# Kernel tuning notes

Measured on AMD Instinct MI355X. Metric: run time of the kernel, lower is better.

The kernel has to match this reference:

```python
import jax, jax.numpy as jnp
import numpy as np

NUM_HEADS = 16
ROPE_BASE = 10000.0


def _rope_interleaved(x, cos, sin):
    # x: (B, S, H, hd); cos/sin: (1, S, 1, hd//2)
    x1 = x[..., ::2]
    x2 = x[..., 1::2]
    r1 = x1 * cos - x2 * sin
    r2 = x1 * sin + x2 * cos
    return jnp.stack([r1, r2], axis=-1).reshape(x.shape)


def _rope_tables(seq_len, head_dim, dtype):
    dim = head_dim // 2
    freqs = jnp.exp(-jnp.arange(0, dim, dtype=dtype) * jnp.log(jnp.asarray(ROPE_BASE, dtype)) / dim)
    pos = jnp.arange(seq_len, dtype=dtype)
    angles = pos[:, None] * freqs[None, :]  # (S, hd//2)
    return jnp.cos(angles)[None, :, None, :], jnp.sin(angles)[None, :, None, :]


def setup_inputs() -> dict:
    key = jax.random.key(0)
    ks = jax.random.split(key, 9)
    B, S, D = 2, 2048, 2048
    sc = 1.0 / np.sqrt(D)
    return {
        "x": jax.random.normal(ks[0], (B, S, D), jnp.float32),
        "wq": jax.random.normal(ks[1], (D, D), jnp.float32) * sc,
        "bq": jax.random.normal(ks[2], (D,), jnp.float32) * 0.01,
        "wk": jax.random.normal(ks[3], (D, D), jnp.float32) * sc,
        "bk": jax.random.normal(ks[4], (D,), jnp.float32) * 0.01,
        "wv": jax.random.normal(ks[5], (D, D), jnp.float32) * sc,
        "bv": jax.random.normal(ks[6], (D,), jnp.float32) * 0.01,
        "wo": jax.random.normal(ks[7], (D, D), jnp.float32) * sc,
        "bo": jax.random.normal(ks[8], (D,), jnp.float32) * 0.01,
    }


def reference(x, wq, bq, wk, bk, wv, bv, wo, bo):
    B, S, D = x.shape
    H = NUM_HEADS
    hd = D // H
    # QKV projections (eqx.nn.Linear: y = W @ x + b, weight (out, in))
    q = (x @ wq.T + bq).reshape(B, S, H, hd)
    k = (x @ wk.T + bk).reshape(B, S, H, hd)
    v = (x @ wv.T + bv).reshape(B, S, H, hd)
    # RoPE (interleaved / GPT-NeoX style)
    cos, sin = _rope_tables(S, hd, x.dtype)
    q = _rope_interleaved(q, cos, sin)
    k = _rope_interleaved(k, cos, sin)
    # Causal scaled dot-product attention
    scale = 1.0 / np.sqrt(hd)
    scores = jnp.einsum("bqhd,bkhd->bhqk", q, k) * scale
    causal = jnp.tril(jnp.ones((S, S), dtype=bool))
    scores = jnp.where(causal[None, None, :, :], scores, jnp.finfo(scores.dtype).min)
    attn = jax.nn.softmax(scores, axis=-1)
    out = jnp.einsum("bhqk,bkhd->bqhd", attn, v).reshape(B, S, D)
    return out @ wo.T + bo
```

## Files before the change

### kernel.cpp

```cpp
#include <hip/hip_runtime.h>

typedef unsigned short u16;
typedef short bf16x8 __attribute__((ext_vector_type(8)));
typedef float f32x4 __attribute__((ext_vector_type(4)));

#define B_ 2
#define S_ 2048
#define D_ 2048
#define HD_ 128
#define GW 512
#define KB 64
#define VST 72
#define PST 72

__device__ __forceinline__ float bf2f(u16 h) {
  unsigned u = ((unsigned)h) << 16;
  return __builtin_bit_cast(float, u);
}
__device__ __forceinline__ u16 f2bf(float f) {
  unsigned u = __builtin_bit_cast(unsigned, f);
  u += 0x7FFF + ((u >> 16) & 1);
  return (u16)(u >> 16);
}
__device__ __forceinline__ bf16x8 cvt8(const float* p) {
  float4 a = *(const float4*)p;
  float4 b = *(const float4*)(p + 4);
  bf16x8 r;
  r[0] = (short)f2bf(a.x); r[1] = (short)f2bf(a.y);
  r[2] = (short)f2bf(a.z); r[3] = (short)f2bf(a.w);
  r[4] = (short)f2bf(b.x); r[5] = (short)f2bf(b.y);
  r[6] = (short)f2bf(b.z); r[7] = (short)f2bf(b.w);
  return r;
}

__device__ __forceinline__ void gload16(const void* g, void* lds) {
  __builtin_amdgcn_global_load_lds(
      (const __attribute__((address_space(1))) unsigned*)g,
      (__attribute__((address_space(3))) unsigned*)lds, 16, 0, 0);
}

__device__ __forceinline__ f32x4 mfma16(bf16x8 a, bf16x8 b, f32x4 c) {
  return __builtin_amdgcn_mfma_f32_16x16x32_bf16(a, b, c, 0, 0, 0);
}

__global__ void k_cvt_all(const float* __restrict__ x, const float* __restrict__ wq,
                          const float* __restrict__ wk, const float* __restrict__ wv,
                          const float* __restrict__ wo, u16* __restrict__ xb,
                          u16* __restrict__ wqkvb, u16* wob, float2* tab) {
  const int slice = blockIdx.y;
  const int i = blockIdx.x * 256 + threadIdx.x;
  if (slice == 5) {
    if (tab != nullptr && i < 131072) {
      const int s = i >> 6, ip = i & 63;
      const float freq = expf(-(float)ip * 0.14391157f);
      float sv, cv;
      sincosf((float)s * freq, &sv, &cv);
      tab[i] = make_float2(cv, sv);
    }
    return;
  }
  if (slice == 4 && wob == nullptr) return;
  const float* src;
  u16* dst;
  int n8;
  if (slice == 0) { src = x; dst = xb; n8 = 1048576; }
  else if (slice == 1) { src = wq; dst = wqkvb; n8 = 524288; }
  else if (slice == 2) { src = wk; dst = wqkvb + 4194304; n8 = 524288; }
  else if (slice == 3) { src = wv; dst = wqkvb + 8388608; n8 = 524288; }
  else { src = wo; dst = wob; n8 = 524288; }
  if (i < n8) *(bf16x8*)(dst + (size_t)i * 8) = cvt8(src + (size_t)i * 8);
}

__global__ __launch_bounds__(512, 2) void k_gemm_qkv_256(
    const u16* __restrict__ xb, const u16* __restrict__ wqkvb,
    const float* __restrict__ bq, const float* __restrict__ bk,
    const float* __restrict__ bv, u16* __restrict__ q, u16* __restrict__ k,
    u16* __restrict__ v, const float2* __restrict__ tab) {
  constexpr int K = 2048, NT = 32;
  __shared__ u16 SA[2][256 * 64];
  __shared__ u16 SB[2][256 * 64];
  const int z = blockIdx.z;
  const u16* W = wqkvb + (size_t)z * D_ * D_;
  const float* bias = z == 0 ? bq : (z == 1 ? bk : bv);
  u16* C = z == 0 ? q : (z == 1 ? k : v);
  const float2* tb = z == 2 ? nullptr : tab;

  const int t = threadIdx.x, wid = t >> 6, l = t & 63, lr = l & 15, lg = l >> 4;
  const int wm = wid >> 2, wn = wid & 3;
  const int m0 = blockIdx.y * 256, n0 = blockIdx.x * 256;

  const int srow = wid * 8 + (l >> 3);
  const int sc = (l & 7) ^ (srow & 7);

  f32x4 acc[8][4];
#pragma unroll
  for (int i = 0; i < 8; ++i)
#pragma unroll
    for (int j = 0; j < 4; ++j) acc[i][j] = f32x4{0.f, 0.f, 0.f, 0.f};

#pragma unroll
  for (int r = 0; r < 4; ++r) {
    const int row = r * 64 + srow;
    gload16(xb + (size_t)(m0 + row) * K + sc * 8,
            (void*)(SA[0] + (size_t)(r * 64 + wid * 8) * 64));
    gload16(W + (size_t)(n0 + row) * K + sc * 8,
            (void*)(SB[0] + (size_t)(r * 64 + wid * 8) * 64));
  }
  asm volatile("s_waitcnt vmcnt(0)" ::: "memory");
  __builtin_amdgcn_sched_barrier(0);
  __builtin_amdgcn_s_barrier();
  __builtin_amdgcn_sched_barrier(0);

  for (int tt = 0; tt < NT; ++tt) {
    const int slot = tt & 1;
    if (tt + 1 < NT) {
      const int kt = (tt + 1) * 64;
#pragma unroll
      for (int r = 0; r < 4; ++r) {
        const int row = r * 64 + srow;
        gload16(xb + (size_t)(m0 + row) * K + kt + sc * 8,
                (void*)(SA[slot ^ 1] + (size_t)(r * 64 + wid * 8) * 64));
        gload16(W + (size_t)(n0 + row) * K + kt + sc * 8,
                (void*)(SB[slot ^ 1] + (size_t)(r * 64 + wid * 8) * 64));
      }
    }
    const u16* sa = SA[slot];
    const u16* sb = SB[slot];
#pragma unroll
    for (int ks = 0; ks < 2; ++ks) {
      const int ch = ((ks * 4 + lg) ^ (lr & 7)) * 8;
      bf16x8 bf[4], af[8];
#pragma unroll
      for (int j = 0; j < 4; ++j)
        bf[j] = *(const bf16x8*)(sb + (size_t)(wn * 64 + j * 16 + lr) * 64 + ch);
#pragma unroll
      for (int i = 0; i < 8; ++i)
        af[i] = *(const bf16x8*)(sa + (size_t)(wm * 128 + i * 16 + lr) * 64 + ch);
      __builtin_amdgcn_s_setprio(1);
#pragma unroll
      for (int i = 0; i < 8; ++i)
#pragma unroll
        for (int j = 0; j < 4; ++j)
          acc[i][j] = mfma16(af[i], bf[j], acc[i][j]);
      __builtin_amdgcn_s_setprio(0);
    }
    asm volatile("s_waitcnt vmcnt(0)" ::: "memory");
    __builtin_amdgcn_sched_barrier(0);
    __builtin_amdgcn_s_barrier();
    __builtin_amdgcn_sched_barrier(0);
  }

#pragma unroll
  for (int i = 0; i < 8; ++i) {
#pragma unroll
    for (int j = 0; j < 4; ++j) {
      const int col = n0 + wn * 64 + j * 16 + lr;
      const float bv_ = bias[col];
      const int row = m0 + wm * 128 + i * 16 + lg * 4;
      if (tb != nullptr) {
        const int ip = (col & 127) >> 1;
        const int odd = col & 1;
#pragma unroll
        for (int r = 0; r < 4; ++r) {
          const float vv = acc[i][j][r] + bv_;
          const float pp = __shfl_xor(vv, 1, 64);
          const float2 cs = tb[((row + r) & (S_ - 1)) * 64 + ip];
          const float o = odd ? (pp * cs.y + vv * cs.x) : (vv * cs.x - pp * cs.y);
          C[(size_t)(row + r) * D_ + col] = f2bf(o);
        }
      } else {
#pragma unroll
        for (int r = 0; r < 4; ++r)
          C[(size_t)(row + r) * D_ + col] = f2bf(acc[i][j][r] + bv_);
      }
    }
  }
}

template <int AM, int WM, int CM>
__device__ __forceinline__ void gemm_body(const void* Ap, const void* Wp,
                                          const float* __restrict__ bias,
                                          void* Cp, int ldc) {
  constexpr int K = 2048;
  __shared__ u16 As[128 * 32];
  __shared__ u16 Bs[128 * 32];
  const int t = threadIdx.x;
  const int w = t >> 6, l = t & 63, lr = l & 15, lg = l >> 4;
  const int m0 = blockIdx.y * 128, n0 = blockIdx.x * 128;
  const int wr = w >> 1, wc = w & 1;

  f32x4 acc[4][4];
#pragma unroll
  for (int i = 0; i < 4; ++i)
#pragma unroll
    for (int j = 0; j < 4; ++j) acc[i][j] = f32x4{0.f, 0.f, 0.f, 0.f};

  const int rowA0 = t >> 2, ko0 = (t & 3) * 8;
  const int rowA1 = (t + 256) >> 2, ko1 = ((t + 256) & 3) * 8;

  for (int kt = 0; kt < K; kt += 32) {
    if constexpr (AM == 1) {
      const u16* A = (const u16*)Ap;
      gload16(A + (size_t)(m0 + rowA0) * K + kt + ko0, (char*)As + (size_t)w * 1024);
      gload16(A + (size_t)(m0 + rowA1) * K + kt + ko1, (char*)As + (size_t)(w + 4) * 1024);
    } else {
      const float* A = (const float*)Ap;
      *(bf16x8*)((char*)As + (size_t)t * 16) = cvt8(A + (size_t)(m0 + rowA0) * K + kt + ko0);
      *(bf16x8*)((char*)As + (size_t)(t + 256) * 16) = cvt8(A + (size_t)(m0 + rowA1) * K + kt + ko1);
    }
    if constexpr (WM == 1) {
      const u16* W = (const u16*)Wp;
      gload16(W + (size_t)(n0 + rowA0) * K + kt + ko0, (char*)Bs + (size_t)w * 1024);
      gload16(W + (size_t)(n0 + rowA1) * K + kt + ko1, (char*)Bs + (size_t)(w + 4) * 1024);
    } else {
      const float* W = (const float*)Wp;
      *(bf16x8*)((char*)Bs + (size_t)t * 16) = cvt8(W + (size_t)(n0 + rowA0) * K + kt + ko0);
      *(bf16x8*)((char*)Bs + (size_t)(t + 256) * 16) = cvt8(W + (size_t)(n0 + rowA1) * K + kt + ko1);
    }
    __syncthreads();

    bf16x8 af[4], bw[4];
#pragma unroll
    for (int i = 0; i < 4; ++i) {
      af[i] = *(const bf16x8*)(As + (size_t)(wr * 64 + i * 16 + lr) * 32 + lg * 8);
      bw[i] = *(const bf16x8*)(Bs + (size_t)(wc * 64 + i * 16 + lr) * 32 + lg * 8);
    }
#pragma unroll
    for (int i = 0; i < 4; ++i)
#pragma unroll
      for (int j = 0; j < 4; ++j)
        acc[i][j] = mfma16(af[i], bw[j], acc[i][j]);
    __syncthreads();
  }

#pragma unroll
  for (int i = 0; i < 4; ++i) {
#pragma unroll
    for (int j = 0; j < 4; ++j) {
      const int col = n0 + wc * 64 + j * 16 + lr;
      const float bv = bias[col];
      const int row = m0 + wr * 64 + i * 16 + lg * 4;
#pragma unroll
      for (int r = 0; r < 4; ++r) {
        if constexpr (CM == 1)
          ((float*)Cp)[(size_t)(row + r) * ldc + col] = acc[i][j][r] + bv;
        else
          ((u16*)Cp)[(size_t)(row + r) * ldc + col] = f2bf(acc[i][j][r] + bv);
      }
    }
  }
}

__global__ __launch_bounds__(256) void k_gemm_out_bb(
    const u16* __restrict__ ao, const u16* __restrict__ wob,
    const float* __restrict__ bo, float* __restrict__ out) {
  gemm_body<1, 1, 1>(ao, wob, bo, out, D_);
}

__global__ __launch_bounds__(256) void k_gemm_qkv_xb(
    const u16* __restrict__ xb, const float* __restrict__ wq,
    const float* __restrict__ bq, const float* __restrict__ wk,
    const float* __restrict__ bk, const float* __restrict__ wv,
    const float* __restrict__ bv, u16* __restrict__ q, u16* __restrict__ k,
    u16* __restrict__ v) {
  const int z = blockIdx.z;
  const float* W = z == 0 ? wq : (z == 1 ? wk : wv);
  const float* bias = z == 0 ? bq : (z == 1 ? bk : bv);
  u16* C = z == 0 ? q : (z == 1 ? k : v);
  gemm_body<1, 0, 0>(xb, W, bias, C, D_);
}

__global__ __launch_bounds__(256) void k_gemm_out(const u16* __restrict__ ao,
                                                  const float* __restrict__ wo,
                                                  const float* __restrict__ bo,
                                                  float* __restrict__ out) {
  gemm_body<1, 0, 1>(ao, wo, bo, out, D_);
}

__global__ __launch_bounds__(256) void k_gemm_qkv_g(
    const float* __restrict__ x, const float* __restrict__ wq,
    const float* __restrict__ bq, const float* __restrict__ wk,
    const float* __restrict__ bk, const float* __restrict__ wv,
    const float* __restrict__ bv, u16* __restrict__ qg, u16* __restrict__ kg,
    u16* __restrict__ vg, int g) {
  const int z = blockIdx.z;
  const float* W = (z == 0 ? wq : (z == 1 ? wk : wv)) + (size_t)g * GW * D_;
  const float* bias = (z == 0 ? bq : (z == 1 ? bk : bv)) + g * GW;
  u16* C = z == 0 ? qg : (z == 1 ? kg : vg);
  gemm_body<0, 0, 0>(x, W, bias, C, GW);
}

__device__ __forceinline__ void rope_one(u16* p, float cv, float sv) {
  unsigned u = *(const unsigned*)p;
  float x1 = bf2f((u16)(u & 0xffff)), x2 = bf2f((u16)(u >> 16));
  unsigned r = (unsigned)f2bf(x1 * cv - x2 * sv) |
               ((unsigned)f2bf(x1 * sv + x2 * cv) << 16);
  *(unsigned*)p = r;
}

__global__ void k_rope_full(u16* q, u16* kk) {
  const int idx = blockIdx.x * 256 + threadIdx.x;
  const int i = idx & 63;
  const int hh = (idx >> 6) & 15;
  const int bs = idx >> 10;
  const int s = bs & (S_ - 1);
  const float freq = expf(-(float)i * 0.14391157f);
  float sv, cv;
  sincosf((float)s * freq, &sv, &cv);
  const size_t off = (size_t)bs * D_ + (size_t)hh * HD_ + 2 * i;
  rope_one(q + off, cv, sv);
  rope_one(kk + off, cv, sv);
}

__global__ void k_rope_g(u16* q, u16* kk) {
  const int idx = blockIdx.x * 256 + threadIdx.x;
  const int i = idx & 63;
  const int hh = (idx >> 6) & 3;
  const int bs = idx >> 8;
  const int s = bs & (S_ - 1);
  const float freq = expf(-(float)i * 0.14391157f);
  float sv, cv;
  sincosf((float)s * freq, &sv, &cv);
  const size_t off = (size_t)bs * GW + (size_t)hh * HD_ + 2 * i;
  rope_one(q + off, cv, sv);
  rope_one(kk + off, cv, sv);
}

__device__ __forceinline__ void attn_body(const u16* Q, const u16* Kd,
                                          const u16* V, u16* O,
                                          size_t base_in, size_t base_out,
                                          int ld_in, int ld_out, int q0) {
  const int t = threadIdx.x, w = t >> 6, l = t & 63, lr = l & 15, lg = l >> 4;

  __shared__ u16 Ks[2][KB * HD_];
  __shared__ u16 Vt[2][HD_ * VST];
  __shared__ u16 Ps[4][16 * PST];

  bf16x8 qf[4];
  {
    const u16* qp = Q + base_in + (size_t)(q0 + w * 16 + lr) * ld_in;
#pragma unroll
    for (int ds = 0; ds < 4; ++ds)
      qf[ds] = *(const bf16x8*)(qp + ds * 32 + lg * 8);
  }

  f32x4 oacc[8];
#pragma unroll
  for (int f = 0; f < 8; ++f) oacc[f] = f32x4{0.f, 0.f, 0.f, 0.f};
  float mrow = -1e30f, lrow = 0.f;

  const int qrow = q0 + w * 16 + lr;
  const int nt = q0 / KB + 1;
  const float sc = 0.08838834764831845f;

  const int c1 = t + 256;
  const int kk20 = (t & 31) * 2, d00 = (t >> 5) * 8;
  const int kk21 = (c1 & 31) * 2, d01 = (c1 >> 5) * 8;

  bf16x8 vc[4];

#pragma unroll
  for (int r = 0; r < 4; ++r) {
    const int c = t + 256 * r;
    const int row = c >> 4, c16 = c & 15;
    const int gc = c16 ^ (row & 7);
    gload16(Kd + base_in + (size_t)row * ld_in + gc * 8,
            (char*)Ks[0] + (size_t)(w + 4 * r) * 1024);
  }
  vc[0] = *(const bf16x8*)(V + base_in + (size_t)kk20 * ld_in + d00);
  vc[1] = *(const bf16x8*)(V + base_in + (size_t)(kk20 + 1) * ld_in + d00);
  vc[2] = *(const bf16x8*)(V + base_in + (size_t)kk21 * ld_in + d01);
  vc[3] = *(const bf16x8*)(V + base_in + (size_t)(kk21 + 1) * ld_in + d01);

  for (int tt = 0; tt < nt; ++tt) {
    const int cur = tt & 1;
    const int kv0 = tt * KB;
    const bool more = (tt + 1 < nt);

    if (more) {
      const int kvn = kv0 + KB;
#pragma unroll
      for (int r = 0; r < 4; ++r) {
        const int c = t + 256 * r;
        const int row = c >> 4, c16 = c & 15;
        const int gc = c16 ^ (row & 7);
        gload16(Kd + base_in + (size_t)(kvn + row) * ld_in + gc * 8,
                (char*)Ks[cur ^ 1] + (size_t)(w + 4 * r) * 1024);
      }
      asm volatile("s_waitcnt vmcnt(4)" ::: "memory");
    } else {
      asm volatile("s_waitcnt vmcnt(0)" ::: "memory");
    }
    __builtin_amdgcn_sched_barrier(0);

    {
      u16* vt = Vt[cur];
#pragma unroll
      for (int j = 0; j < 8; ++j) {
        unsigned p0 = (unsigned)(unsigned short)vc[0][j] |
                      ((unsigned)(unsigned short)vc[1][j] << 16);
        *(unsigned*)&vt[(size_t)(d00 + j) * VST + kk20] = p0;
        unsigned p1 = (unsigned)(unsigned short)vc[2][j] |
                      ((unsigned)(unsigned short)vc[3][j] << 16);
        *(unsigned*)&vt[(size_t)(d01 + j) * VST + kk21] = p1;
      }
    }
    if (more) {
      const int kvn = kv0 + KB;
      vc[0] = *(const bf16x8*)(V + base_in + (size_t)(kvn + kk20) * ld_in + d00);
      vc[1] = *(const bf16x8*)(V + base_in + (size_t)(kvn + kk20 + 1) * ld_in + d00);
      vc[2] = *(const bf16x8*)(V + base_in + (size_t)(kvn + kk21) * ld_in + d01);
      vc[3] = *(const bf16x8*)(V + base_in + (size_t)(kvn + kk21 + 1) * ld_in + d01);
    }
    asm volatile("s_waitcnt lgkmcnt(0)" ::: "memory");
    __builtin_amdgcn_sched_barrier(0);
    __builtin_amdgcn_s_barrier();
    __builtin_amdgcn_sched_barrier(0);

    float p[16];
    __builtin_amdgcn_s_setprio(1);
#pragma unroll
    for (int h = 0; h < 4; ++h) {
      f32x4 s = {0.f, 0.f, 0.f, 0.f};
#pragma unroll
      for (int ds = 0; ds < 4; ++ds) {
        const int ch = (ds * 4 + lg) ^ (lr & 7);
        bf16x8 kf = *(const bf16x8*)(Ks[cur] + (size_t)(h * 16 + lr) * HD_ + ch * 8);
        s = mfma16(kf, qf[ds], s);
      }
#pragma unroll
      for (int r = 0; r < 4; ++r) p[h * 4 + r] = s[r] * sc;
    }
    __builtin_amdgcn_s_setprio(0);
    if (kv0 + KB - 1 > q0 + w * 16) {
#pragma unroll
      for (int h = 0; h < 4; ++h)
#pragma unroll
        for (int r = 0; r < 4; ++r)
          if (kv0 + h * 16 + lg * 4 + r > qrow) p[h * 4 + r] = -1e30f;
    }
    float pm = p[0];
#pragma unroll
    for (int i = 1; i < 16; ++i) pm = fmaxf(pm, p[i]);
    pm = fmaxf(pm, __shfl_xor(pm, 16, 64));
    pm = fmaxf(pm, __shfl_xor(pm, 32, 64));
    const float mn = fmaxf(mrow, pm);
    const float scl = __expf(mrow - mn);
    mrow = mn;
    float rs = 0.f;
#pragma unroll
    for (int i = 0; i < 16; ++i) {
      p[i] = __expf(p[i] - mn);
      rs += p[i];
    }
    rs += __shfl_xor(rs, 16, 64);
    rs += __shfl_xor(rs, 32, 64);
    lrow = lrow * scl + rs;
    float sj[4];
#pragma unroll
    for (int j = 0; j < 4; ++j) sj[j] = __shfl(scl, lg * 4 + j, 64);
#pragma unroll
    for (int f = 0; f < 8; ++f)
#pragma unroll
      for (int j = 0; j < 4; ++j) oacc[f][j] *= sj[j];
#pragma unroll
    for (int h = 0; h < 4; ++h)
#pragma unroll
      for (int r = 0; r < 4; ++r)
        Ps[w][lr * PST + h * 16 + lg * 4 + r] = f2bf(p[h * 4 + r]);
    bf16x8 pf0 = *(const bf16x8*)&Ps[w][lr * PST + lg * 8];
    bf16x8 pf1 = *(const bf16x8*)&Ps[w][lr * PST + 32 + lg * 8];
    __builtin_amdgcn_s_setprio(1);
#pragma unroll
    for (int f = 0; f < 8; ++f) {
      bf16x8 vf0 = *(const bf16x8*)&Vt[cur][(size_t)(f * 16 + lr) * VST + lg * 8];
      bf16x8 vf1 = *(const bf16x8*)&Vt[cur][(size_t)(f * 16 + lr) * VST + 32 + lg * 8];
      oacc[f] = mfma16(pf0, vf0, oacc[f]);
      oacc[f] = mfma16(pf1, vf1, oacc[f]);
    }
    __builtin_amdgcn_s_setprio(0);
    __builtin_amdgcn_sched_barrier(0);
    __builtin_amdgcn_s_barrier();
    __builtin_amdgcn_sched_barrier(0);
  }

  const float inv = 1.0f / lrow;
  float ij[4];
#pragma unroll
  for (int j = 0; j < 4; ++j) ij[j] = __shfl(inv, lg * 4 + j, 64);
  u16* Op = O + base_out;
#pragma unroll
  for (int f = 0; f < 8; ++f)
#pragma unroll
    for (int j = 0; j < 4; ++j)
      Op[(size_t)(q0 + w * 16 + lg * 4 + j) * ld_out + f * 16 + lr] =
          f2bf(oacc[f][j] * ij[j]);
}

__global__ __launch_bounds__(256) void k_attn_full(const u16* Q, const u16* Kd,
                                                   const u16* V, u16* O) {
  const int lin = blockIdx.y * gridDim.x + blockIdx.x;
  const int work = (lin & 7) * 64 + (lin >> 3);
  const int bh = work >> 4;
  const int pr = work & 15;
  const int b = bh >> 4, h = bh & 15;
  const size_t base = ((size_t)b * S_) * D_ + (size_t)h * HD_;
  attn_body(Q, Kd, V, O, base, base, D_, D_, 64 * (31 - pr));
  attn_body(Q, Kd, V, O, base, base, D_, D_, 64 * pr);
}

__global__ __launch_bounds__(256) void k_attn_g(const u16* __restrict__ Q,
                                                const u16* __restrict__ Kd,
                                                const u16* __restrict__ V,
                                                u16* __restrict__ O, int g) {
  const int by = blockIdx.y;
  const int b = by >> 2, hh = by & 3;
  const size_t base_in = ((size_t)b * S_) * GW + (size_t)hh * HD_;
  const size_t base_out = ((size_t)b * S_) * D_ + (size_t)(g * 4 + hh) * HD_;
  attn_body(Q, Kd, V, O, base_in, base_out, GW, D_, blockIdx.x * 64);
}

extern "C" void kernel_launch(void* const* d_in, const int* in_sizes, int n_in,
                              void* d_out, int out_size, void* d_ws,
                              size_t ws_size, hipStream_t stream) {
  (void)in_sizes; (void)n_in; (void)out_size;
  const float* x = (const float*)d_in[0];
  const float* wq = (const float*)d_in[1];
  const float* bq = (const float*)d_in[2];
  const float* wk = (const float*)d_in[3];
  const float* bk = (const float*)d_in[4];
  const float* wv = (const float*)d_in[5];
  const float* bv = (const float*)d_in[6];
  const float* wo = (const float*)d_in[7];
  const float* bo = (const float*)d_in[8];
  float* out = (float*)d_out;

  const size_t XB = (size_t)B_ * S_ * D_ * 2;
  const size_t WB3 = 3 * (size_t)D_ * D_ * 2;
  const size_t WB1 = (size_t)D_ * D_ * 2;
  const size_t TB = (size_t)S_ * 64 * 8;
  char* ws = (char*)d_ws;
  char* ob = (char*)d_out;

  u16 *xb, *q, *k, *v, *wqkvb = nullptr, *wob = nullptr;
  float2* tab = nullptr;
  int tier;
  if (ws_size >= 4 * XB + WB3 + WB1 + TB) {
    xb = (u16*)ws; q = (u16*)(ws + XB); k = (u16*)(ws + 2 * XB);
    v = (u16*)(ws + 3 * XB);
    wqkvb = (u16*)(ws + 4 * XB); wob = (u16*)(ws + 4 * XB + WB3);
    tab = (float2*)(ws + 4 * XB + WB3 + WB1);
    tier = 1;
  } else if (ws_size >= 3 * XB + WB3 + WB1 + TB) {
    xb = (u16*)ob;
    q = (u16*)ws; k = (u16*)(ws + XB); v = (u16*)(ws + 2 * XB);
    wqkvb = (u16*)(ws + 3 * XB); wob = (u16*)(ws + 3 * XB + WB3);
    tab = (float2*)(ws + 3 * XB + WB3 + WB1);
    tier = 1;
  } else if (ws_size >= 2 * XB + WB3 + TB) {
    xb = (u16*)ob; v = (u16*)(ob + XB);
    q = (u16*)ws; k = (u16*)(ws + XB);
    wqkvb = (u16*)(ws + 2 * XB);
    tab = (float2*)(ws + 2 * XB + WB3);
    tier = 2;
  } else if (ws_size >= 2 * XB) {
    xb = (u16*)ob; v = (u16*)(ob + XB);
    q = (u16*)ws; k = (u16*)(ws + XB);
    tier = 3;
  } else {
    tier = 4;
  }

  if (tier == 1 || tier == 2) {
    dim3 gc(4096, 6);
    k_cvt_all<<<gc, 256, 0, stream>>>(x, wq, wk, wv, wo, xb, wqkvb, wob, tab);
    dim3 g1(8, 16, 3);
    k_gemm_qkv_256<<<g1, 512, 0, stream>>>(xb, wqkvb, bq, bk, bv, q, k, v, tab);
    dim3 g2(16, 32);
    k_attn_full<<<g2, 256, 0, stream>>>(q, k, v, q);
    dim3 g3(16, 32);
    if (tier == 1)
      k_gemm_out_bb<<<g3, 256, 0, stream>>>(q, wob, bo, out);
    else
      k_gemm_out<<<g3, 256, 0, stream>>>(q, wo, bo, out);
  } else if (tier == 3) {
    dim3 gc(4096, 1);
    k_cvt_all<<<gc, 256, 0, stream>>>(x, wq, wk, wv, wo, xb, xb, nullptr, nullptr);
    dim3 g1(16, 32, 3);
    k_gemm_qkv_xb<<<g1, 256, 0, stream>>>(xb, wq, bq, wk, bk, wv, bv, q, k, v);
    k_rope_full<<<16384, 256, 0, stream>>>(q, k);
    dim3 g2(16, 32);
    k_attn_full<<<g2, 256, 0, stream>>>(q, k, v, q);
    dim3 g3(16, 32);
    k_gemm_out<<<g3, 256, 0, stream>>>(q, wo, bo, out);
  } else {
    u16* qg = (u16*)ob;
    u16* kg = qg + (size_t)(B_ * S_) * GW;
    u16* vg = kg + (size_t)(B_ * S_) * GW;
    u16* ao = (u16*)ws;
    for (int g = 0; g < 4; ++g) {
      dim3 g1(4, 32, 3);
      k_gemm_qkv_g<<<g1, 256, 0, stream>>>(x, wq, bq, wk, bk, wv, bv, qg, kg, vg, g);
      k_rope_g<<<4096, 256, 0, stream>>>(qg, kg);
      dim3 g2(32, 8);
      k_attn_g<<<g2, 256, 0, stream>>>(qg, kg, vg, ao, g);
    }
    dim3 g3(16, 32);
    k_gemm_out<<<g3, 256, 0, stream>>>(ao, wo, bo, out);
  }
}
```

Baseline: 298.7 us.

## Split GEMM k-step into four phases interleaving LDS reads, global prefetch, and MFMA

Restructures the projection GEMM main loop into four quarter phases, each loading a subset of A/B fragments from LDS and issuing 16 MFMAs, with the global prefetch of the next A and B tiles spread across the first two phases. Extra workgroup barriers are inserted between phases so waves line up their LDS reads and MFMA bursts. The aim is to overlap LDS and global memory traffic with matrix math and to cut the registers held for B fragments. The cost is that the re-read A fragments (loaded twice per ks) add LDS traffic, and the extra barriers may stall waves.

Result: no change. 298.7 us (+0.0%).

```diff
diff --git a/kernel.cpp b/kernel.cpp
--- a/kernel.cpp
+++ b/kernel.cpp
@@ -111,44 +111,71 @@
   __builtin_amdgcn_s_barrier();
   __builtin_amdgcn_sched_barrier(0);
 
+#define LOADQ(ks, jh)                                                          \
+  {                                                                            \
+    const int ch8 = (((ks)*4 + lg) ^ (lr & 7)) * 8;                            \
+    _Pragma("unroll") for (int i = 0; i < 8; ++i) af[i] =                      \
+        *(const bf16x8*)(sa + (size_t)(wm * 128 + i * 16 + lr) * 64 + ch8);    \
+    _Pragma("unroll") for (int jj = 0; jj < 2; ++jj) bf[jj] =                  \
+        *(const bf16x8*)(sb + (size_t)(wn * 64 + ((jh)*2 + jj) * 16 + lr) * 64 \
+                         + ch8);                                               \
+  }
+#define MFMAQ(jh)                                                              \
+  asm volatile("s_waitcnt lgkmcnt(0)" ::: "memory");                           \
+  __builtin_amdgcn_sched_barrier(0);                                           \
+  __builtin_amdgcn_s_setprio(1);                                               \
+  _Pragma("unroll") for (int i = 0; i < 8; ++i)                                \
+      _Pragma("unroll") for (int jj = 0; jj < 2; ++jj)                         \
+          acc[i][(jh)*2 + jj] = mfma16(af[i], bf[jj], acc[i][(jh)*2 + jj]);    \
+  __builtin_amdgcn_s_setprio(0);                                               \
+  __builtin_amdgcn_sched_barrier(0);
+
   for (int tt = 0; tt < NT; ++tt) {
     const int slot = tt & 1;
-    if (tt + 1 < NT) {
-      const int kt = (tt + 1) * 64;
-#pragma unroll
-      for (int r = 0; r < 4; ++r) {
-        const int row = r * 64 + srow;
-        gload16(xb + (size_t)(m0 + row) * K + kt + sc * 8,
-                (void*)(SA[slot ^ 1] + (size_t)(r * 64 + wid * 8) * 64));
-        gload16(W + (size_t)(n0 + row) * K + kt + sc * 8,
-                (void*)(SB[slot ^ 1] + (size_t)(r * 64 + wid * 8) * 64));
-      }
-    }
     const u16* sa = SA[slot];
     const u16* sb = SB[slot];
-#pragma unroll
-    for (int ks = 0; ks < 2; ++ks) {
-      const int ch = ((ks * 4 + lg) ^ (lr & 7)) * 8;
-      bf16x8 bf[4], af[8];
-#pragma unroll
-      for (int j = 0; j < 4; ++j)
-        bf[j] = *(const bf16x8*)(sb + (size_t)(wn * 64 + j * 16 + lr) * 64 + ch);
-#pragma unroll
-      for (int i = 0; i < 8; ++i)
-        af[i] = *(const bf16x8*)(sa + (size_t)(wm * 128 + i * 16 + lr) * 64 + ch);
-      __builtin_amdgcn_s_setprio(1);
-#pragma unroll
-      for (int i = 0; i < 8; ++i)
-#pragma unroll
-        for (int j = 0; j < 4; ++j)
-          acc[i][j] = mfma16(af[i], bf[j], acc[i][j]);
-      __builtin_amdgcn_s_setprio(0);
-    }
+    u16* da = SA[slot ^ 1];
+    u16* db = SB[slot ^ 1];
+    const bool more = (tt + 1 < NT);
+    const int kt = (tt + 1) * 64;
+    bf16x8 af[8], bf[2];
+
+    LOADQ(0, 0);
+    if (more) {
+#pragma unroll
+      for (int r = 0; r < 4; ++r)
+        gload16(xb + (size_t)(m0 + r * 64 + srow) * K + kt + sc * 8,
+                (void*)(da + (size_t)(r * 64 + wid * 8) * 64));
+    }
+    __builtin_amdgcn_s_barrier();
+    MFMAQ(0);
+    __builtin_amdgcn_s_barrier();
+
+    LOADQ(1, 0);
+    if (more) {
+#pragma unroll
+      for (int r = 0; r < 4; ++r)
+        gload16(W + (size_t)(n0 + r * 64 + srow) * K + kt + sc * 8,
+                (void*)(db + (size_t)(r * 64 + wid * 8) * 64));
+    }
+    __builtin_amdgcn_s_barrier();
+    MFMAQ(0);
+    __builtin_amdgcn_s_barrier();
+
+    LOADQ(0, 1);
+    __builtin_amdgcn_s_barrier();
+    MFMAQ(1);
+    __builtin_amdgcn_s_barrier();
+
+    LOADQ(1, 1);
     asm volatile("s_waitcnt vmcnt(0)" ::: "memory");
     __builtin_amdgcn_sched_barrier(0);
     __builtin_amdgcn_s_barrier();
-    __builtin_amdgcn_sched_barrier(0);
-  }
+    MFMAQ(1);
+    __builtin_amdgcn_s_barrier();
+  }
+#undef LOADQ
+#undef MFMAQ
 
 #pragma unroll
   for (int i = 0; i < 8; ++i) {
```
